# Performance work log

Hardware: AMD Instinct MI355X
Metric: run time of the kernel (lower is better)

## Reference

```python
import jax, jax.numpy as jnp
import numpy as np

TEMPERATURE = 0.07
WEIGHT = 0.5
EPS = 1e-8  # torch CosineSimilarity eps


def setup_inputs() -> dict:
    key = jax.random.key(0)
    k1, k2 = jax.random.split(key)
    N, D = 16384, 256
    img_features = jax.random.normal(k1, (N, D), dtype=jnp.float32)
    txt_features = jax.random.normal(k2, (N, D), dtype=jnp.float32)
    return {"img_features": img_features, "txt_features": txt_features}


def _l2_normalize(x):
    # matches torch cosine_similarity: clamp each norm to EPS
    n = jnp.sqrt(jnp.sum(x * x, axis=-1, keepdims=True))
    return x / jnp.maximum(n, EPS)


def reference(img_features, txt_features):
    v = _l2_normalize(img_features)  # [N, D]
    u = _l2_normalize(txt_features)  # [N, D]
    # cosine-sim matrix via GEMM (same math as broadcasted CosineSimilarity)
    sim_vu = jnp.einsum('nd,md->nm', v, u) / TEMPERATURE  # [N, N]
    sim_uv = sim_vu.T  # cosine similarity is symmetric in its args
    N = sim_vu.shape[0]
    diag = jnp.arange(N)
    # CrossEntropyLoss with targets = arange(N): mean over rows of -log_softmax[i, i]
    logp_vu = jax.nn.log_softmax(sim_vu, axis=-1)
    logp_uv = jax.nn.log_softmax(sim_uv, axis=-1)
    loss_vu = -jnp.mean(logp_vu[diag, diag])
    loss_uv = -jnp.mean(logp_uv[diag, diag])
    total = WEIGHT * loss_vu + (1.0 - WEIGHT) * loss_uv
    # corresponds to {'T': total, 'I-T': loss_vu, 'T-I': loss_uv}
    return jnp.stack([total, loss_vu, loss_uv])
```

## Files before the change

### kernel.cpp

```cpp
#include <hip/hip_runtime.h>
#include <hip/hip_bf16.h>


#define D_DIM 256

constexpr float INV_T = 1.0f / 0.07f;
constexpr float EXP2_SCALE = 1.44269504088896340736f / 0.07f;

typedef __bf16 bf16x8 __attribute__((ext_vector_type(8)));
typedef float f32x4 __attribute__((ext_vector_type(4)));

__global__ __launch_bounds__(256) void normalize_kernel(
    const float* __restrict__ img, const float* __restrict__ txt,
    __hip_bfloat16* __restrict__ Vf, __hip_bfloat16* __restrict__ Uf,
    float* __restrict__ diagarr, float* __restrict__ rowsum,
    float* __restrict__ colsum) {
  const int wave = threadIdx.x >> 6;
  const int lane = threadIdx.x & 63;
  const int sub = lane >> 5;
  const int pos = lane & 31;
  const int row = blockIdx.x * 8 + wave * 2 + sub;
  const size_t base = (size_t)row * D_DIM + pos * 8;

  const float4 i0 = *reinterpret_cast<const float4*>(&img[base]);
  const float4 i1 = *reinterpret_cast<const float4*>(&img[base + 4]);
  const float4 t0 = *reinterpret_cast<const float4*>(&txt[base]);
  const float4 t1 = *reinterpret_cast<const float4*>(&txt[base + 4]);

  float a = i0.x * i0.x + i0.y * i0.y + i0.z * i0.z + i0.w * i0.w +
            i1.x * i1.x + i1.y * i1.y + i1.z * i1.z + i1.w * i1.w;
  float b = t0.x * t0.x + t0.y * t0.y + t0.z * t0.z + t0.w * t0.w +
            t1.x * t1.x + t1.y * t1.y + t1.z * t1.z + t1.w * t1.w;
#pragma unroll
  for (int off = 1; off < 32; off <<= 1) {
    a += __shfl_xor(a, off, 64);
    b += __shfl_xor(b, off, 64);
  }
  const float si = 1.0f / fmaxf(sqrtf(a), 1e-8f);
  const float st = 1.0f / fmaxf(sqrtf(b), 1e-8f);

  const float vs = si * EXP2_SCALE;
  __hip_bfloat16 vb8[8] = {
      __float2bfloat16(i0.x * vs), __float2bfloat16(i0.y * vs),
      __float2bfloat16(i0.z * vs), __float2bfloat16(i0.w * vs),
      __float2bfloat16(i1.x * vs), __float2bfloat16(i1.y * vs),
      __float2bfloat16(i1.z * vs), __float2bfloat16(i1.w * vs)};
  __hip_bfloat16 ub8[8] = {
      __float2bfloat16(t0.x * st), __float2bfloat16(t0.y * st),
      __float2bfloat16(t0.z * st), __float2bfloat16(t0.w * st),
      __float2bfloat16(t1.x * st), __float2bfloat16(t1.y * st),
      __float2bfloat16(t1.z * st), __float2bfloat16(t1.w * st)};

  const int g = row >> 4, l15r = row & 15;
  const int ks = pos >> 2, quad = pos & 3;
  const size_t foff = (size_t)(g * 8 + ks) * 512 + (quad * 16 + l15r) * 8;
  *reinterpret_cast<uint4*>(&Vf[foff]) = *reinterpret_cast<uint4*>(vb8);
  *reinterpret_cast<uint4*>(&Uf[foff]) = *reinterpret_cast<uint4*>(ub8);

  float d = (i0.x * si) * (t0.x * st) + (i0.y * si) * (t0.y * st) +
            (i0.z * si) * (t0.z * st) + (i0.w * si) * (t0.w * st) +
            (i1.x * si) * (t1.x * st) + (i1.y * si) * (t1.y * st) +
            (i1.z * si) * (t1.z * st) + (i1.w * si) * (t1.w * st);
#pragma unroll
  for (int off = 1; off < 32; off <<= 1) d += __shfl_xor(d, off, 64);
  if (pos == 0) diagarr[row] = d;

  if (threadIdx.x < 8) {
    rowsum[blockIdx.x * 8 + threadIdx.x] = 0.0f;
    colsum[blockIdx.x * 8 + threadIdx.x] = 0.0f;
  }
}

__global__ __launch_bounds__(512, 2) void gemm_lse_kernel(
    const __hip_bfloat16* __restrict__ Vf, const __hip_bfloat16* __restrict__ Uf,
    float* __restrict__ rowsum, float* __restrict__ colsum, int n) {
  const int tid = threadIdx.x;
  const int lane = tid & 63;
  const int w = tid >> 6;
  const int quad = lane >> 4;
  const int l15 = lane & 15;
  const int b = blockIdx.x;
  const int njt = n >> 9;

  bf16x8 a[4][8];
#pragma unroll
  for (int mi = 0; mi < 4; ++mi)
#pragma unroll
    for (int ks = 0; ks < 8; ++ks)
      a[mi][ks] = *reinterpret_cast<const bf16x8*>(
          Vf + (size_t)((4 * b + mi) * 8 + ks) * 512 + lane * 8);

  float rs[4][4] = {};

  const __hip_bfloat16* Ub = Uf + (size_t)(w * 4) * 8 * 512 + lane * 8;

  bf16x8 bb[2][4];
#pragma unroll
  for (int ni = 0; ni < 4; ++ni)
    bb[0][ni] = *reinterpret_cast<const bf16x8*>(Ub + (size_t)(ni * 8) * 512);

  for (int jt = 0; jt < njt; ++jt) {
    const size_t jb = (size_t)jt * (32 * 8 * 512);
    const size_t jbn = (jt < njt - 1) ? jb + 32 * 8 * 512 : 0;
    f32x4 acc[4][4] = {};

#pragma unroll
    for (int ks = 0; ks < 8; ++ks) {
      {
        const size_t pjb = (ks < 7) ? jb : jbn;
        const int pks = (ks < 7) ? ks + 1 : 0;
#pragma unroll
        for (int ni = 0; ni < 4; ++ni)
          bb[(ks + 1) & 1][ni] = *reinterpret_cast<const bf16x8*>(
              Ub + pjb + (size_t)(ni * 8 + pks) * 512);
        __builtin_amdgcn_sched_barrier(0);
      }
#pragma unroll
      for (int mi = 0; mi < 4; ++mi)
#pragma unroll
        for (int ni = 0; ni < 4; ++ni)
          acc[mi][ni] = __builtin_amdgcn_mfma_f32_16x16x32_bf16(
              a[mi][ks], bb[ks & 1][ni], acc[mi][ni], 0, 0, 0);
    }

    float cs0 = 0.f, cs1 = 0.f, cs2 = 0.f, cs3 = 0.f;
#pragma unroll
    for (int mi = 0; mi < 4; ++mi)
#pragma unroll
      for (int r = 0; r < 4; ++r) {
        const float e0 = __builtin_amdgcn_exp2f(acc[mi][0][r]);
        const float e1 = __builtin_amdgcn_exp2f(acc[mi][1][r]);
        const float e2 = __builtin_amdgcn_exp2f(acc[mi][2][r]);
        const float e3 = __builtin_amdgcn_exp2f(acc[mi][3][r]);
        rs[mi][r] += e0 + e1 + e2 + e3;
        cs0 += e0; cs1 += e1; cs2 += e2; cs3 += e3;
      }
    float csa[4] = {cs0, cs1, cs2, cs3};
#pragma unroll
    for (int ni = 0; ni < 4; ++ni) {
      float c = csa[ni];
      c += __shfl_xor(c, 16, 64);
      c += __shfl_xor(c, 32, 64);
      if (lane < 16)
        atomicAdd(&colsum[jt * 512 + w * 64 + ni * 16 + l15], c);
    }
  }

#pragma unroll
  for (int mi = 0; mi < 4; ++mi)
#pragma unroll
    for (int r = 0; r < 4; ++r) {
      float v = rs[mi][r];
      v += __shfl_xor(v, 1, 64);
      v += __shfl_xor(v, 2, 64);
      v += __shfl_xor(v, 4, 64);
      v += __shfl_xor(v, 8, 64);
      if (l15 == 0)
        atomicAdd(&rowsum[b * 64 + mi * 16 + quad * 4 + r], v);
    }
}

__global__ __launch_bounds__(1024) void finalize_kernel(
    const float* __restrict__ rowsum, const float* __restrict__ colsum,
    const float* __restrict__ diagarr, float* __restrict__ out, int n) {
  __shared__ float sh[48];
  float sr = 0.0f, sc = 0.0f, sd = 0.0f;
  for (int i = threadIdx.x; i < n; i += 1024) {
    sr += __logf(rowsum[i]);
    sc += __logf(colsum[i]);
    sd += diagarr[i];
  }
#pragma unroll
  for (int off = 1; off < 64; off <<= 1) {
    sr += __shfl_xor(sr, off, 64);
    sc += __shfl_xor(sc, off, 64);
    sd += __shfl_xor(sd, off, 64);
  }
  const int w = threadIdx.x >> 6, lane = threadIdx.x & 63;
  if (lane == 0) { sh[w] = sr; sh[16 + w] = sc; sh[32 + w] = sd; }
  __syncthreads();
  if (threadIdx.x == 0) {
    float tr = 0.0f, tc = 0.0f, td = 0.0f;
#pragma unroll
    for (int i = 0; i < 16; ++i) {
      tr += sh[i]; tc += sh[16 + i]; td += sh[32 + i];
    }
    const float invN = 1.0f / (float)n;
    const float dm = td * INV_T * invN;
    const float lvu = tr * invN - dm;
    const float luv = tc * invN - dm;
    out[0] = 0.5f * lvu + 0.5f * luv;
    out[1] = lvu;
    out[2] = luv;
  }
}

extern "C" void kernel_launch(void* const* d_in, const int* in_sizes, int n_in,
                              void* d_out, int out_size, void* d_ws, size_t ws_size,
                              hipStream_t stream) {
  const float* img = (const float*)d_in[0];
  const float* txt = (const float*)d_in[1];
  float* out = (float*)d_out;
  const int N = in_sizes[0] / D_DIM;

  char* ws = (char*)d_ws;
  __hip_bfloat16* Vf = (__hip_bfloat16*)ws;
  __hip_bfloat16* Uf = (__hip_bfloat16*)(ws + (size_t)N * D_DIM * 2);
  float* rowsum = (float*)(ws + (size_t)N * D_DIM * 4);
  float* colsum = rowsum + N;
  float* diagarr = colsum + N;

  normalize_kernel<<<N / 8, 256, 0, stream>>>(img, txt, Vf, Uf, diagarr,
                                              rowsum, colsum);

  gemm_lse_kernel<<<N / 64, 512, 0, stream>>>(Vf, Uf, rowsum, colsum, N);

  finalize_kernel<<<1, 1024, 0, stream>>>(rowsum, colsum, diagarr, out, N);
}
```

Measured before the change: 223.1 us.

## Buffer column sums in shared memory and parallelize final reduction

Column partial sums are stored in a per-block shared-memory buffer instead of being atomically added to global memory after every column tile. Each block then flushes the whole buffer with one pass of global atomics. The single-block finalize kernel is replaced by a 64-block partial reduction using atomics plus a tiny scalar kernel. The fixed 16384-entry shared buffer ties the kernel to N at most 16384, and the large LDS use may limit occupancy.

```diff
diff --git a/kernel.cpp b/kernel.cpp
--- a/kernel.cpp
+++ b/kernel.cpp
@@ -14,7 +14,7 @@
     const float* __restrict__ img, const float* __restrict__ txt,
     __hip_bfloat16* __restrict__ Vf, __hip_bfloat16* __restrict__ Uf,
     float* __restrict__ diagarr, float* __restrict__ rowsum,
-    float* __restrict__ colsum) {
+    float* __restrict__ colsum, float* __restrict__ partials) {
   const int wave = threadIdx.x >> 6;
   const int lane = threadIdx.x & 63;
   const int sub = lane >> 5;
@@ -69,11 +69,14 @@
     rowsum[blockIdx.x * 8 + threadIdx.x] = 0.0f;
     colsum[blockIdx.x * 8 + threadIdx.x] = 0.0f;
   }
+  if (blockIdx.x == 0 && threadIdx.x < 4) partials[threadIdx.x] = 0.0f;
 }
 
 __global__ __launch_bounds__(512, 2) void gemm_lse_kernel(
     const __hip_bfloat16* __restrict__ Vf, const __hip_bfloat16* __restrict__ Uf,
     float* __restrict__ rowsum, float* __restrict__ colsum, int n) {
+  __shared__ float colbuf[16384];
+
   const int tid = threadIdx.x;
   const int lane = tid & 63;
   const int w = tid >> 6;
@@ -142,9 +145,12 @@
       c += __shfl_xor(c, 16, 64);
       c += __shfl_xor(c, 32, 64);
       if (lane < 16)
-        atomicAdd(&colsum[jt * 512 + w * 64 + ni * 16 + l15], c);
+        colbuf[jt * 512 + w * 64 + ni * 16 + l15] = c;
     }
   }
+
+  __syncthreads();
+  for (int i = tid; i < n; i += 512) atomicAdd(&colsum[i], colbuf[i]);
 
 #pragma unroll
   for (int mi = 0; mi < 4; ++mi)
@@ -160,12 +166,11 @@
     }
 }
 
-__global__ __launch_bounds__(1024) void finalize_kernel(
+__global__ __launch_bounds__(256) void finalize_partial(
     const float* __restrict__ rowsum, const float* __restrict__ colsum,
-    const float* __restrict__ diagarr, float* __restrict__ out, int n) {
-  __shared__ float sh[48];
+    const float* __restrict__ diagarr, float* __restrict__ partials, int n) {
   float sr = 0.0f, sc = 0.0f, sd = 0.0f;
-  for (int i = threadIdx.x; i < n; i += 1024) {
+  for (int i = blockIdx.x * 256 + threadIdx.x; i < n; i += gridDim.x * 256) {
     sr += __logf(rowsum[i]);
     sc += __logf(colsum[i]);
     sd += diagarr[i];
@@ -176,23 +181,22 @@
     sc += __shfl_xor(sc, off, 64);
     sd += __shfl_xor(sd, off, 64);
   }
-  const int w = threadIdx.x >> 6, lane = threadIdx.x & 63;
-  if (lane == 0) { sh[w] = sr; sh[16 + w] = sc; sh[32 + w] = sd; }
-  __syncthreads();
-  if (threadIdx.x == 0) {
-    float tr = 0.0f, tc = 0.0f, td = 0.0f;
-#pragma unroll
-    for (int i = 0; i < 16; ++i) {
-      tr += sh[i]; tc += sh[16 + i]; td += sh[32 + i];
-    }
-    const float invN = 1.0f / (float)n;
-    const float dm = td * INV_T * invN;
-    const float lvu = tr * invN - dm;
-    const float luv = tc * invN - dm;
-    out[0] = 0.5f * lvu + 0.5f * luv;
-    out[1] = lvu;
-    out[2] = luv;
-  }
+  if ((threadIdx.x & 63) == 0) {
+    atomicAdd(&partials[0], sr);
+    atomicAdd(&partials[1], sc);
+    atomicAdd(&partials[2], sd);
+  }
+}
+
+__global__ void finalize_final(const float* __restrict__ partials,
+                               float* __restrict__ out, int n) {
+  const float invN = 1.0f / (float)n;
+  const float dm = partials[2] * INV_T * invN;
+  const float lvu = partials[0] * invN - dm;
+  const float luv = partials[1] * invN - dm;
+  out[0] = 0.5f * lvu + 0.5f * luv;
+  out[1] = lvu;
+  out[2] = luv;
 }
 
 extern "C" void kernel_launch(void* const* d_in, const int* in_sizes, int n_in,
@@ -209,11 +213,14 @@
   float* rowsum = (float*)(ws + (size_t)N * D_DIM * 4);
   float* colsum = rowsum + N;
   float* diagarr = colsum + N;
+  float* partials = diagarr + N;
 
   normalize_kernel<<<N / 8, 256, 0, stream>>>(img, txt, Vf, Uf, diagarr,
-                                              rowsum, colsum);
+                                              rowsum, colsum, partials);
 
   gemm_lse_kernel<<<N / 64, 512, 0, stream>>>(Vf, Uf, rowsum, colsum, N);
 
-  finalize_kernel<<<1, 1024, 0, stream>>>(rowsum, colsum, diagarr, out, N);
-}
+  finalize_partial<<<64, 256, 0, stream>>>(rowsum, colsum, diagarr, partials,
+                                           N);
+  finalize_final<<<1, 1, 0, stream>>>(partials, out, N);
+}
```

New measurement: 234.0 us. +4.9%, slower.

## Fuse finalize into GEMM via last-block reduction and in-block row sums

Applied to the files above, without the earlier changes.

Removes the separate single-block finalize kernel. Row sums are now reduced in shared memory per block and logged locally, and the diagonal sum is accumulated with one atomic per normalize block. The last GEMM block, found with an atomic counter, reduces the column sums and writes the outputs. This cuts a kernel launch and a serial 1024-thread pass, but adds a memset, a threadfence, and a serial tail in one block.

```diff
diff --git a/kernel.cpp b/kernel.cpp
--- a/kernel.cpp
+++ b/kernel.cpp
@@ -13,10 +13,12 @@
 __global__ __launch_bounds__(256) void normalize_kernel(
     const float* __restrict__ img, const float* __restrict__ txt,
     __hip_bfloat16* __restrict__ Vf, __hip_bfloat16* __restrict__ Uf,
-    float* __restrict__ diagarr, float* __restrict__ rowsum,
-    float* __restrict__ colsum) {
-  const int wave = threadIdx.x >> 6;
-  const int lane = threadIdx.x & 63;
+    float* __restrict__ colsum, float* __restrict__ partials) {
+  __shared__ float shd[4];
+
+  const int t = threadIdx.x;
+  const int wave = t >> 6;
+  const int lane = t & 63;
   const int sub = lane >> 5;
   const int pos = lane & 31;
   const int row = blockIdx.x * 8 + wave * 2 + sub;
@@ -31,10 +33,13 @@
             i1.x * i1.x + i1.y * i1.y + i1.z * i1.z + i1.w * i1.w;
   float b = t0.x * t0.x + t0.y * t0.y + t0.z * t0.z + t0.w * t0.w +
             t1.x * t1.x + t1.y * t1.y + t1.z * t1.z + t1.w * t1.w;
+  float d = i0.x * t0.x + i0.y * t0.y + i0.z * t0.z + i0.w * t0.w +
+            i1.x * t1.x + i1.y * t1.y + i1.z * t1.z + i1.w * t1.w;
 #pragma unroll
   for (int off = 1; off < 32; off <<= 1) {
     a += __shfl_xor(a, off, 64);
     b += __shfl_xor(b, off, 64);
+    d += __shfl_xor(d, off, 64);
   }
   const float si = 1.0f / fmaxf(sqrtf(a), 1e-8f);
   const float st = 1.0f / fmaxf(sqrtf(b), 1e-8f);
@@ -57,23 +62,23 @@
   *reinterpret_cast<uint4*>(&Vf[foff]) = *reinterpret_cast<uint4*>(vb8);
   *reinterpret_cast<uint4*>(&Uf[foff]) = *reinterpret_cast<uint4*>(ub8);
 
-  float d = (i0.x * si) * (t0.x * st) + (i0.y * si) * (t0.y * st) +
-            (i0.z * si) * (t0.z * st) + (i0.w * si) * (t0.w * st) +
-            (i1.x * si) * (t1.x * st) + (i1.y * si) * (t1.y * st) +
-            (i1.z * si) * (t1.z * st) + (i1.w * si) * (t1.w * st);
-#pragma unroll
-  for (int off = 1; off < 32; off <<= 1) d += __shfl_xor(d, off, 64);
-  if (pos == 0) diagarr[row] = d;
-
-  if (threadIdx.x < 8) {
-    rowsum[blockIdx.x * 8 + threadIdx.x] = 0.0f;
-    colsum[blockIdx.x * 8 + threadIdx.x] = 0.0f;
-  }
+  float dn = d * si * st;
+  dn += __shfl_xor(dn, 32, 64);
+  if (lane == 0) shd[wave] = dn;
+  __syncthreads();
+  if (t == 0) atomicAdd(&partials[2], shd[0] + shd[1] + shd[2] + shd[3]);
+
+  if (t < 8) colsum[blockIdx.x * 8 + t] = 0.0f;
 }
 
 __global__ __launch_bounds__(512, 2) void gemm_lse_kernel(
     const __hip_bfloat16* __restrict__ Vf, const __hip_bfloat16* __restrict__ Uf,
-    float* __restrict__ rowsum, float* __restrict__ colsum, int n) {
+    float* __restrict__ colsum, float* __restrict__ partials,
+    float* __restrict__ out, int n) {
+  __shared__ float rowbuf[64];
+  __shared__ float shred[8];
+  __shared__ unsigned s_last;
+
   const int tid = threadIdx.x;
   const int lane = tid & 63;
   const int w = tid >> 6;
@@ -146,6 +151,8 @@
     }
   }
 
+  if (tid < 64) rowbuf[tid] = 0.0f;
+  __syncthreads();
 #pragma unroll
   for (int mi = 0; mi < 4; ++mi)
 #pragma unroll
@@ -156,42 +163,44 @@
       v += __shfl_xor(v, 4, 64);
       v += __shfl_xor(v, 8, 64);
       if (l15 == 0)
-        atomicAdd(&rowsum[b * 64 + mi * 16 + quad * 4 + r], v);
-    }
-}
-
-__global__ __launch_bounds__(1024) void finalize_kernel(
-    const float* __restrict__ rowsum, const float* __restrict__ colsum,
-    const float* __restrict__ diagarr, float* __restrict__ out, int n) {
-  __shared__ float sh[48];
-  float sr = 0.0f, sc = 0.0f, sd = 0.0f;
-  for (int i = threadIdx.x; i < n; i += 1024) {
-    sr += __logf(rowsum[i]);
-    sc += __logf(colsum[i]);
-    sd += diagarr[i];
-  }
-#pragma unroll
-  for (int off = 1; off < 64; off <<= 1) {
-    sr += __shfl_xor(sr, off, 64);
-    sc += __shfl_xor(sc, off, 64);
-    sd += __shfl_xor(sd, off, 64);
-  }
-  const int w = threadIdx.x >> 6, lane = threadIdx.x & 63;
-  if (lane == 0) { sh[w] = sr; sh[16 + w] = sc; sh[32 + w] = sd; }
-  __syncthreads();
-  if (threadIdx.x == 0) {
-    float tr = 0.0f, tc = 0.0f, td = 0.0f;
-#pragma unroll
-    for (int i = 0; i < 16; ++i) {
-      tr += sh[i]; tc += sh[16 + i]; td += sh[32 + i];
-    }
-    const float invN = 1.0f / (float)n;
-    const float dm = td * INV_T * invN;
-    const float lvu = tr * invN - dm;
-    const float luv = tc * invN - dm;
-    out[0] = 0.5f * lvu + 0.5f * luv;
-    out[1] = lvu;
-    out[2] = luv;
+        atomicAdd(&rowbuf[mi * 16 + quad * 4 + r], v);
+    }
+  __syncthreads();
+  if (tid < 64) {
+    float lg = __logf(rowbuf[tid]);
+#pragma unroll
+    for (int off = 1; off < 64; off <<= 1) lg += __shfl_xor(lg, off, 64);
+    if (tid == 0) atomicAdd(&partials[0], lg);
+  }
+
+  __threadfence();
+  if (tid == 0) {
+    const unsigned old = atomicAdd((unsigned*)(partials + 3), 1u);
+    s_last = (old == (unsigned)(gridDim.x - 1)) ? 1u : 0u;
+  }
+  __syncthreads();
+  if (s_last) {
+    float sc = 0.0f;
+    for (int i = tid; i < n; i += 512)
+      sc += __logf(atomicAdd(&colsum[i], 0.0f));
+#pragma unroll
+    for (int off = 1; off < 64; off <<= 1) sc += __shfl_xor(sc, off, 64);
+    if (lane == 0) shred[w] = sc;
+    __syncthreads();
+    if (tid == 0) {
+      float tc = 0.0f;
+#pragma unroll
+      for (int i = 0; i < 8; ++i) tc += shred[i];
+      const float sr = atomicAdd(&partials[0], 0.0f);
+      const float td = atomicAdd(&partials[2], 0.0f);
+      const float invN = 1.0f / (float)n;
+      const float dm = td * INV_T * invN;
+      const float lvu = sr * invN - dm;
+      const float luv = tc * invN - dm;
+      out[0] = 0.5f * lvu + 0.5f * luv;
+      out[1] = lvu;
+      out[2] = luv;
+    }
   }
 }
 
@@ -206,14 +215,14 @@
   char* ws = (char*)d_ws;
   __hip_bfloat16* Vf = (__hip_bfloat16*)ws;
   __hip_bfloat16* Uf = (__hip_bfloat16*)(ws + (size_t)N * D_DIM * 2);
-  float* rowsum = (float*)(ws + (size_t)N * D_DIM * 4);
-  float* colsum = rowsum + N;
-  float* diagarr = colsum + N;
-
-  normalize_kernel<<<N / 8, 256, 0, stream>>>(img, txt, Vf, Uf, diagarr,
-                                              rowsum, colsum);
-
-  gemm_lse_kernel<<<N / 64, 512, 0, stream>>>(Vf, Uf, rowsum, colsum, N);
-
-  finalize_kernel<<<1, 1024, 0, stream>>>(rowsum, colsum, diagarr, out, N);
+  float* colsum = (float*)(ws + (size_t)N * D_DIM * 4);
+  float* partials = colsum + N;
+
+  hipMemsetAsync(partials, 0, 4 * sizeof(float), stream);
+
+  normalize_kernel<<<N / 8, 256, 0, stream>>>(img, txt, Vf, Uf, colsum,
+                                              partials);
+
+  gemm_lse_kernel<<<N / 64, 512, 0, stream>>>(Vf, Uf, colsum, partials, out,
+                                              N);
 }
```

Result: slower. 278.4 us (+24.8%).
